# Performance work log

Measured on AMD Instinct MI355X. Metric: run time of the kernel, lower is better.

Reference implementation:

```python
import jax, jax.numpy as jnp
import numpy as np

D_MODEL = 1024
D_STATE = 64
D_CONV = 4
EXPAND = 2
HEADDIM = 64
FFN_MULT = 3
MEM_DIM = 256
D_INNER = EXPAND * D_MODEL            # 2048
NHEADS = D_INNER // HEADDIM           # 32
CONV_DIM = D_INNER + 2 * D_STATE      # x, B, C channels through the causal conv
D_IN_PROJ = 2 * D_INNER + 2 * D_STATE + NHEADS  # z, xBC, dt
FFN_HID = FFN_MULT * D_MODEL


def _rms(x, eps=1e-6):
    return x * jax.lax.rsqrt(jnp.mean(x * x, axis=-1, keepdims=True) + eps)


def _mamba2(u, in_proj_w, conv_w, conv_b, dt_bias, A_log, D_param, mnorm_w, out_proj_w):
    # u: [B, L, d_model]
    Bsz, L, _ = u.shape
    zxbcdt = u @ in_proj_w.T                                  # [B, L, D_IN_PROJ]
    z = zxbcdt[..., :D_INNER]                                 # gate branch
    xBC = zxbcdt[..., D_INNER:D_INNER + CONV_DIM]
    dt = zxbcdt[..., D_INNER + CONV_DIM:]                     # [B, L, H]
    # causal depthwise conv1d (kernel D_CONV) + silu
    xp = jnp.pad(xBC, ((0, 0), (D_CONV - 1, 0), (0, 0)))
    xBC = sum(xp[:, k:k + L, :] * conv_w[:, k] for k in range(D_CONV)) + conv_b
    xBC = jax.nn.silu(xBC)
    xh = xBC[..., :D_INNER].reshape(Bsz, L, NHEADS, HEADDIM)  # [B, L, H, P]
    Bm = xBC[..., D_INNER:D_INNER + D_STATE]                  # [B, L, N] (ngroups=1)
    Cm = xBC[..., D_INNER + D_STATE:]                         # [B, L, N]
    dt = jax.nn.softplus(dt + dt_bias)                        # [B, L, H]
    dA = jnp.exp(dt * (-jnp.exp(A_log)))                      # [B, L, H]

    def step(h, inp):
        # h: [B, H, P, N]
        da, dtt, xt, bt, ct = inp
        h = da[:, :, None, None] * h + jnp.einsum('bh,bhp,bn->bhpn', dtt, xt, bt)
        y = jnp.einsum('bhpn,bn->bhp', h, ct)
        return h, y

    h0 = jnp.zeros((Bsz, NHEADS, HEADDIM, D_STATE), u.dtype)
    xs = (jnp.moveaxis(dA, 1, 0), jnp.moveaxis(dt, 1, 0), jnp.moveaxis(xh, 1, 0),
          jnp.moveaxis(Bm, 1, 0), jnp.moveaxis(Cm, 1, 0))
    _, ys = jax.lax.scan(step, h0, xs)                        # ys: [L, B, H, P]
    y = jnp.moveaxis(ys, 0, 1) + D_param[None, None, :, None] * xh
    y = y.reshape(Bsz, L, D_INNER)
    y = _rms(y * jax.nn.silu(z)) * mnorm_w                    # RMSNormGated
    return y @ out_proj_w.T


def setup_inputs() -> dict:
    key = jax.random.key(0)
    ks = jax.random.split(key, 12)
    B, L = 1, 2048
    s = 0.02
    return {
        'x': jax.random.normal(ks[0], (B, L, D_MODEL), jnp.float32),
        'x0': jax.random.normal(ks[1], (B, L, D_MODEL), jnp.float32),
        'mem': jax.random.normal(ks[2], (B, MEM_DIM), jnp.float32),
        'resid_mix': jnp.stack([jnp.ones(D_MODEL), jnp.zeros(D_MODEL)]),
        'ssm_scale': jnp.ones(D_MODEL),
        'mlp_scale': jnp.ones(D_MODEL),
        'ssm_norm_w': jnp.ones(D_MODEL),
        'ffn_norm_w': jnp.ones(D_MODEL),
        'in_proj_w': jax.random.normal(ks[3], (D_IN_PROJ, D_MODEL), jnp.float32) * s,
        'conv_w': jax.random.normal(ks[4], (CONV_DIM, D_CONV), jnp.float32) * 0.2,
        'conv_b': jnp.zeros(CONV_DIM),
        'dt_bias': jax.random.uniform(ks[5], (NHEADS,), jnp.float32, -2.0, 0.0),
        'A_log': jnp.log(jnp.linspace(1.0, 16.0, NHEADS).astype(jnp.float32)),
        'D_param': jnp.ones(NHEADS),
        'mnorm_w': jnp.ones(D_INNER),
        'out_proj_w': jax.random.normal(ks[6], (D_MODEL, D_INNER), jnp.float32) * s,
        'gate_up_w': jax.random.normal(ks[7], (2 * FFN_HID, D_MODEL), jnp.float32) * s,
        'down_w': jax.random.normal(ks[8], (D_MODEL, FFN_HID), jnp.float32) * s,
    }


def reference(x, x0, mem, resid_mix, ssm_scale, mlp_scale, ssm_norm_w, ffn_norm_w,
              in_proj_w, conv_w, conv_b, dt_bias, A_log, D_param, mnorm_w,
              out_proj_w, gate_up_w, down_w):
    # residual mixing (USE_MEMORY=0, so mem path is inert)
    x = resid_mix[0][None, None, :] * x + resid_mix[1][None, None, :] * x0
    y = _mamba2(_rms(x) * ssm_norm_w, in_proj_w, conv_w, conv_b, dt_bias,
                A_log, D_param, mnorm_w, out_proj_w)
    x = x + ssm_scale[None, None, :] * y
    # SwiGLU FFN
    h = _rms(x) * ffn_norm_w
    gu = h @ gate_up_w.T
    gate, up = jnp.split(gu, 2, axis=-1)
    x = x + mlp_scale[None, None, :] * ((jax.nn.silu(gate) * up) @ down_w.T)
    return x
```

## Files before the change

kernel.cpp:

```cpp
#include <hip/hip_runtime.h>
#include <hip/hip_bf16.h>
#include <math.h>

#define LSEQ 2048
#define DMODEL 1024
#define DINNER 2048
#define NHEADS 32
#define HEADDIM 64
#define DSTATE 64
#define CONVDIM 2176
#define XBCDT_W 2304
#define FFNHID 3072

typedef float f32x4 __attribute__((ext_vector_type(4)));
typedef __bf16 bf16x8 __attribute__((ext_vector_type(8)));
typedef __hip_bfloat16 bf16;

__device__ __forceinline__ float siluf(float x){ return x / (1.0f + expf(-x)); }

#define GLOAD_LDS16(gp, lp) __builtin_amdgcn_global_load_lds( \
    (const __attribute__((address_space(1))) void*)(gp), \
    (__attribute__((address_space(3))) void*)(lp), 16, 0, 0)

__device__ __forceinline__ float block_reduce_sum_256(float v){
  #pragma unroll
  for (int o = 32; o > 0; o >>= 1) v += __shfl_down(v, o, 64);
  __shared__ float sh[4];
  int lane = threadIdx.x & 63;
  int w = threadIdx.x >> 6;
  if (lane == 0) sh[w] = v;
  __syncthreads();
  return sh[0] + sh[1] + sh[2] + sh[3];
}

__device__ __forceinline__ ushort bf16bits(float f){
  __hip_bfloat16 h = __float2bfloat16(f);
  return *reinterpret_cast<ushort*>(&h);
}
__device__ __forceinline__ float bfu(ushort u){
  union { float f; unsigned int i; } w; w.i = ((unsigned int)u) << 16; return w.f;
}

__device__ __forceinline__ int swz64(int r, int c){
  return r*64 + ((((c>>3) ^ (r&7)))<<3) + (c&7);
}

__global__ __launch_bounds__(256) void k_castmix(
    const float* __restrict__ w0, const float* __restrict__ w1,
    const float* __restrict__ w2, const float* __restrict__ w3,
    bf16* __restrict__ d0, bf16* __restrict__ d1,
    bf16* __restrict__ d2, bf16* __restrict__ d3,
    const float* __restrict__ x, const float* __restrict__ x0,
    const float* __restrict__ rm, const float* __restrict__ nw,
    float* __restrict__ xres, bf16* __restrict__ u)
{
  int tid = threadIdx.x;
  if (blockIdx.x < 15616){
    int idx = blockIdx.x * 256 + tid;
    const float* s; bf16* d; int valid;
    if (idx < 1114112)      { s = w0; d = d0; valid = 1089536; }
    else if (idx < 1638400) { idx -= 1114112; s = w1; d = d1; valid = 524288; }
    else if (idx < 3211264) { idx -= 1638400; s = w2; d = d2; valid = 1572864; }
    else                    { idx -= 3211264; s = w3; d = d3; valid = 786432; }
    float4 v = (idx < valid) ? *(const float4*)(s + (size_t)idx * 4)
                             : make_float4(0.f, 0.f, 0.f, 0.f);
    ushort4 r;
    r.x = bf16bits(v.x); r.y = bf16bits(v.y); r.z = bf16bits(v.z); r.w = bf16bits(v.w);
    *(ushort4*)(d + (size_t)idx * 4) = r;
    return;
  }
  int row = blockIdx.x - 15616;
  float4 xv  = ((const float4*)(x  + (size_t)row * DMODEL))[tid];
  float4 x0v = ((const float4*)(x0 + (size_t)row * DMODEL))[tid];
  float4 r0 = ((const float4*)rm)[tid];
  float4 r1 = ((const float4*)(rm + DMODEL))[tid];
  float4 a;
  a.x = r0.x*xv.x + r1.x*x0v.x; a.y = r0.y*xv.y + r1.y*x0v.y;
  a.z = r0.z*xv.z + r1.z*x0v.z; a.w = r0.w*xv.w + r1.w*x0v.w;
  ((float4*)(xres + (size_t)row * DMODEL))[tid] = a;
  float ss = a.x*a.x + a.y*a.y + a.z*a.z + a.w*a.w;
  ss = block_reduce_sum_256(ss);
  float inv = rsqrtf(ss / (float)DMODEL + 1e-6f);
  float4 nv = ((const float4*)nw)[tid];
  ushort4 o;
  o.x = bf16bits(a.x*inv*nv.x); o.y = bf16bits(a.y*inv*nv.y);
  o.z = bf16bits(a.z*inv*nv.z); o.w = bf16bits(a.w*inv*nv.w);
  *(ushort4*)(u + (size_t)row * DMODEL + tid*4) = o;
}

__device__ __forceinline__ void xcdswz2(int &bx, int &by){
  int gx = gridDim.x;
  int nblk = gx * gridDim.y;
  int flat = by * gx + bx;
  flat = (flat & 7) * (nblk >> 3) + (flat >> 3);
  by = flat / gx; bx = flat - by * gx;
}

__device__ __forceinline__ void gemm_mainloop128(
    const bf16* __restrict__ A, const bf16* __restrict__ W,
    int ld, int Klen, bf16* As, bf16* Ws, f32x4 acc[4][4])
{
  int tid = threadIdx.x, lane = tid & 63, wid = tid >> 6;
  int wm = (wid >> 1) * 64, wn = (wid & 1) * 64;
  int r16 = lane & 15, g8 = lane >> 4;
  int srow = lane >> 2;
  int scol = ((lane & 3) ^ (srow & 3) ^ ((srow >> 2) & 3)) * 8;
  const bf16* ga0 = A + (size_t)(wid*32 + srow) * ld + scol;
  const bf16* ga1 = ga0 + (size_t)16 * ld;
  const bf16* gw0 = W + (size_t)(wid*32 + srow) * ld + scol;
  const bf16* gw1 = gw0 + (size_t)16 * ld;
  GLOAD_LDS16(ga0, As + wid*1024);
  GLOAD_LDS16(ga1, As + wid*1024 + 512);
  GLOAD_LDS16(gw0, Ws + wid*1024);
  GLOAD_LDS16(gw1, Ws + wid*1024 + 512);
  __syncthreads();
  int cur = 0;
  int s4 = ((r16 & 3) ^ ((r16 >> 2) & 3)) * 8;
  for (int k0 = 0; k0 < Klen; k0 += 32){
    if (k0 + 32 < Klen){
      int nb = (cur ^ 1) * 4096;
      GLOAD_LDS16(ga0 + k0 + 32, As + nb + wid*1024);
      GLOAD_LDS16(ga1 + k0 + 32, As + nb + wid*1024 + 512);
      GLOAD_LDS16(gw0 + k0 + 32, Ws + nb + wid*1024);
      GLOAD_LDS16(gw1 + k0 + 32, Ws + nb + wid*1024 + 512);
    }
    int cb = cur * 4096;
    bf16x8 af[4], bfr[4];
    #pragma unroll
    for (int i = 0; i < 4; ++i)
      af[i] = *(const bf16x8*)(As + cb + (wm + i*16 + r16)*32 + (g8*8 ^ s4));
    #pragma unroll
    for (int j = 0; j < 4; ++j)
      bfr[j] = *(const bf16x8*)(Ws + cb + (wn + j*16 + r16)*32 + (g8*8 ^ s4));
    #pragma unroll
    for (int i = 0; i < 4; ++i)
      #pragma unroll
      for (int j = 0; j < 4; ++j)
        acc[i][j] = __builtin_amdgcn_mfma_f32_16x16x32_bf16(af[i], bfr[j], acc[i][j], 0, 0, 0);
    __syncthreads();
    cur ^= 1;
  }
}

__global__ __launch_bounds__(256) void k_gemm_inproj(
    const bf16* __restrict__ A, const bf16* __restrict__ Wfull,
    bf16* __restrict__ zbuf, bf16* __restrict__ xbcdt)
{
  __shared__ __align__(16) bf16 As[2*4096];
  __shared__ __align__(16) bf16 Ws[2*4096];
  int bx = blockIdx.x, by = blockIdx.y;
  xcdswz2(bx, by);
  f32x4 acc[4][4];
  #pragma unroll
  for (int i = 0; i < 4; ++i)
    #pragma unroll
    for (int j = 0; j < 4; ++j) acc[i][j] = (f32x4){0.f,0.f,0.f,0.f};
  gemm_mainloop128(A + (size_t)(by*128)*DMODEL, Wfull + (size_t)(bx*128)*DMODEL,
                   DMODEL, DMODEL, As, Ws, acc);
  int tid = threadIdx.x, lane = tid & 63, wid = tid >> 6;
  int wm = (wid >> 1) * 64, wn = (wid & 1) * 64;
  int r16 = lane & 15, g8 = lane >> 4;
  bf16* Cp; int ldc, col0;
  if (bx < 16){ Cp = zbuf;  ldc = DINNER;  col0 = bx*128; }
  else        { Cp = xbcdt; ldc = XBCDT_W; col0 = (bx-16)*128; }
  #pragma unroll
  for (int i = 0; i < 4; ++i){
    int row = by*128 + wm + i*16 + g8*4;
    #pragma unroll
    for (int j = 0; j < 4; ++j){
      int col = col0 + wn + j*16 + r16;
      #pragma unroll
      for (int r = 0; r < 4; ++r)
        Cp[(size_t)(row + r) * ldc + col] = __float2bfloat16(acc[i][j][r]);
    }
  }
}

__global__ __launch_bounds__(256) void k_gemm_splitk(
    const bf16* __restrict__ A, const bf16* __restrict__ W,
    bf16* __restrict__ P, int Kfull, int Kq, int N)
{
  __shared__ __align__(16) bf16 As[2*4096];
  __shared__ __align__(16) bf16 Ws[2*4096];
  int gx = gridDim.x, gxy = gx * gridDim.y;
  int nblk = gxy * gridDim.z;
  int flat = blockIdx.z * gxy + blockIdx.y * gx + blockIdx.x;
  flat = (flat & 7) * (nblk >> 3) + (flat >> 3);
  int z = flat / gxy; int rem = flat - z * gxy;
  int by = rem / gx, bx = rem - by * gx;
  f32x4 acc[4][4];
  #pragma unroll
  for (int i = 0; i < 4; ++i)
    #pragma unroll
    for (int j = 0; j < 4; ++j) acc[i][j] = (f32x4){0.f,0.f,0.f,0.f};
  gemm_mainloop128(A + (size_t)(by*128)*Kfull + z*Kq,
                   W + (size_t)(bx*128)*Kfull + z*Kq,
                   Kfull, Kq, As, Ws, acc);
  bf16* Pz = P + (size_t)z * LSEQ * N;
  int tid = threadIdx.x, lane = tid & 63, wid = tid >> 6;
  int wm = (wid >> 1) * 64, wn = (wid & 1) * 64;
  int r16 = lane & 15, g8 = lane >> 4;
  #pragma unroll
  for (int i = 0; i < 4; ++i){
    int row = by*128 + wm + i*16 + g8*4;
    #pragma unroll
    for (int j = 0; j < 4; ++j){
      int col = bx*128 + wn + j*16 + r16;
      #pragma unroll
      for (int r = 0; r < 4; ++r)
        Pz[(size_t)(row + r) * N + col] = __float2bfloat16(acc[i][j][r]);
    }
  }
}

__global__ __launch_bounds__(256) void k_gemm_ffn(
    const bf16* __restrict__ A, const bf16* __restrict__ Wg, const bf16* __restrict__ Wu,
    bf16* __restrict__ act, int K)
{
  __shared__ __align__(16) bf16 As[2*4096];
  __shared__ __align__(16) bf16 Ws[2*4096];
  int bx = blockIdx.x, by = blockIdx.y;
  xcdswz2(bx, by);
  int tid = threadIdx.x, lane = tid & 63, wid = tid >> 6;
  int wm = (wid >> 1) * 64, wc = (wid & 1) * 32;
  int r16 = lane & 15, g8 = lane >> 4;
  int srow = lane >> 2;
  int scol = ((lane & 3) ^ (srow & 3) ^ ((srow >> 2) & 3)) * 8;
  const bf16* ga0 = A + (size_t)(by*128 + wid*32 + srow) * K + scol;
  const bf16* ga1 = ga0 + (size_t)16 * K;
  const bf16* gwsrc = (wid < 2) ? Wg : Wu;
  const bf16* gw0 = gwsrc + (size_t)(bx*64 + (wid & 1)*32 + srow) * K + scol;
  const bf16* gw1 = gw0 + (size_t)16 * K;
  f32x4 accg[4][2], accu[4][2];
  #pragma unroll
  for (int i = 0; i < 4; ++i)
    #pragma unroll
    for (int j = 0; j < 2; ++j){
      accg[i][j] = (f32x4){0.f,0.f,0.f,0.f};
      accu[i][j] = (f32x4){0.f,0.f,0.f,0.f};
    }
  GLOAD_LDS16(ga0, As + wid*1024);
  GLOAD_LDS16(ga1, As + wid*1024 + 512);
  GLOAD_LDS16(gw0, Ws + wid*1024);
  GLOAD_LDS16(gw1, Ws + wid*1024 + 512);
  __syncthreads();
  int cur = 0;
  int s4 = ((r16 & 3) ^ ((r16 >> 2) & 3)) * 8;
  for (int k0 = 0; k0 < K; k0 += 32){
    if (k0 + 32 < K){
      int nb = (cur ^ 1) * 4096;
      GLOAD_LDS16(ga0 + k0 + 32, As + nb + wid*1024);
      GLOAD_LDS16(ga1 + k0 + 32, As + nb + wid*1024 + 512);
      GLOAD_LDS16(gw0 + k0 + 32, Ws + nb + wid*1024);
      GLOAD_LDS16(gw1 + k0 + 32, Ws + nb + wid*1024 + 512);
    }
    int cb = cur * 4096;
    bf16x8 af[4], gf[2], uf[2];
    #pragma unroll
    for (int i = 0; i < 4; ++i)
      af[i] = *(const bf16x8*)(As + cb + (wm + i*16 + r16)*32 + (g8*8 ^ s4));
    #pragma unroll
    for (int j = 0; j < 2; ++j){
      int gr = wc + j*16 + r16;
      int ur = 64 + wc + j*16 + r16;
      gf[j] = *(const bf16x8*)(Ws + cb + gr*32 + (g8*8 ^ s4));
      uf[j] = *(const bf16x8*)(Ws + cb + ur*32 + (g8*8 ^ s4));
    }
    #pragma unroll
    for (int i = 0; i < 4; ++i)
      #pragma unroll
      for (int j = 0; j < 2; ++j){
        accg[i][j] = __builtin_amdgcn_mfma_f32_16x16x32_bf16(af[i], gf[j], accg[i][j], 0, 0, 0);
        accu[i][j] = __builtin_amdgcn_mfma_f32_16x16x32_bf16(af[i], uf[j], accu[i][j], 0, 0, 0);
      }
    __syncthreads();
    cur ^= 1;
  }
  #pragma unroll
  for (int i = 0; i < 4; ++i){
    int row = by*128 + wm + i*16 + g8*4;
    #pragma unroll
    for (int j = 0; j < 2; ++j){
      int col = bx*64 + wc + j*16 + r16;
      #pragma unroll
      for (int r = 0; r < 4; ++r){
        float g = accg[i][j][r], u = accu[i][j][r];
        act[(size_t)(row + r) * FFNHID + col] = __float2bfloat16(siluf(g) * u);
      }
    }
  }
}

__global__ __launch_bounds__(256) void k_convdt(
    const bf16* __restrict__ xbcdt, const float* __restrict__ cw,
    const float* __restrict__ cb, const float* __restrict__ dtb,
    const float* __restrict__ alog, bf16* __restrict__ xbc,
    float* __restrict__ dtv, float* __restrict__ lav)
{
  int idx = blockIdx.x * 256 + threadIdx.x;
  int l = idx / 552, q = idx - l * 552;
  if (l >= LSEQ) return;
  if (q < 544){
    int c = q * 4;
    float4 bv = *(const float4*)(cb + c);
    float acc0 = bv.x, acc1 = bv.y, acc2 = bv.z, acc3 = bv.w;
    float4 w0 = *(const float4*)(cw + (size_t)(c+0)*4);
    float4 w1 = *(const float4*)(cw + (size_t)(c+1)*4);
    float4 w2 = *(const float4*)(cw + (size_t)(c+2)*4);
    float4 w3 = *(const float4*)(cw + (size_t)(c+3)*4);
    const float* w0p = (const float*)&w0;
    const float* w1p = (const float*)&w1;
    const float* w2p = (const float*)&w2;
    const float* w3p = (const float*)&w3;
    #pragma unroll
    for (int k = 0; k < 4; ++k){
      int t = l + k - 3;
      if (t < 0) continue;
      ushort4 rv = *(const ushort4*)(xbcdt + (size_t)t * XBCDT_W + c);
      acc0 = fmaf(bfu(rv.x), w0p[k], acc0);
      acc1 = fmaf(bfu(rv.y), w1p[k], acc1);
      acc2 = fmaf(bfu(rv.z), w2p[k], acc2);
      acc3 = fmaf(bfu(rv.w), w3p[k], acc3);
    }
    ushort4 o;
    o.x = bf16bits(siluf(acc0)); o.y = bf16bits(siluf(acc1));
    o.z = bf16bits(siluf(acc2)); o.w = bf16bits(siluf(acc3));
    *(ushort4*)(xbc + (size_t)l * CONVDIM + c) = o;
  } else {
    int h0 = (q - 544) * 4;
    ushort4 rv = *(const ushort4*)(xbcdt + (size_t)l * XBCDT_W + CONVDIM + h0);
    float raws[4] = { bfu(rv.x), bfu(rv.y), bfu(rv.z), bfu(rv.w) };
    #pragma unroll
    for (int i = 0; i < 4; ++i){
      float raw = raws[i] + dtb[h0 + i];
      float d = (raw > 20.f) ? raw : log1pf(expf(raw));
      dtv[l * NHEADS + h0 + i] = d;
      lav[l * NHEADS + h0 + i] = -expf(alog[h0 + i]) * d;
    }
  }
}

__global__ __launch_bounds__(256) void k_scanA(
    const bf16* __restrict__ xbc, const float* __restrict__ dtv,
    const float* __restrict__ lav, bf16* __restrict__ T, float* __restrict__ ctot)
{
  __shared__ __bf16 sXw[4096];
  __shared__ __bf16 sBt[4096];
  __shared__ float scum[64], swt[64];
  int h = blockIdx.x >> 5, c = blockIdx.x & 31;
  int tid = threadIdx.x, t0 = c * 64;
  if (tid < 64){
    float cum = lav[(size_t)(t0 + tid) * NHEADS + h];
    #pragma unroll
    for (int o = 1; o < 64; o <<= 1){
      float v = __shfl_up(cum, o, 64);
      if (tid >= o) cum += v;
    }
    scum[tid] = cum;
  }
  __syncthreads();
  float Lc = scum[63];
  if (tid < 64)
    swt[tid] = expf(Lc - scum[tid]) * dtv[(size_t)(t0 + tid) * NHEADS + h];
  __syncthreads();
  for (int idx = tid; idx < 512; idx += 256){
    int j = idx >> 3, n0 = (idx & 7) * 8;
    const bf16* rb = xbc + (size_t)(t0 + j) * CONVDIM;
    bf16x8 x8 = *(const bf16x8*)(rb + h * HEADDIM + n0);
    bf16x8 b8 = *(const bf16x8*)(rb + DINNER + n0);
    float wj = swt[j];
    #pragma unroll
    for (int e = 0; e < 8; ++e){
      sXw[swz64(n0 + e, j)] = (__bf16)((float)x8[e] * wj);
      sBt[swz64(n0 + e, j)] = b8[e];
    }
  }
  __syncthreads();
  int lane = tid & 63, wid = tid >> 6;
  int wr = (wid >> 1) * 32, wc = (wid & 1) * 32;
  int r16 = lane & 15, g8 = lane >> 4;
  f32x4 acc[2][2];
  #pragma unroll
  for (int i = 0; i < 2; ++i)
    #pragma unroll
    for (int j = 0; j < 2; ++j) acc[i][j] = (f32x4){0.f,0.f,0.f,0.f};
  #pragma unroll
  for (int kk = 0; kk < 2; ++kk){
    int ks = kk*4 + g8;
    bf16x8 a[2], b[2];
    #pragma unroll
    for (int i = 0; i < 2; ++i){
      int row = wr + i*16 + r16;
      a[i] = *(const bf16x8*)(sXw + row*64 + ((ks ^ (row&7))<<3));
    }
    #pragma unroll
    for (int j = 0; j < 2; ++j){
      int row = wc + j*16 + r16;
      b[j] = *(const bf16x8*)(sBt + row*64 + ((ks ^ (row&7))<<3));
    }
    #pragma unroll
    for (int i = 0; i < 2; ++i)
      #pragma unroll
      for (int j = 0; j < 2; ++j)
        acc[i][j] = __builtin_amdgcn_mfma_f32_16x16x32_bf16(a[i], b[j], acc[i][j], 0, 0, 0);
  }
  bf16* Tb = T + (size_t)blockIdx.x * 4096;
  #pragma unroll
  for (int i = 0; i < 2; ++i)
    #pragma unroll
    for (int j = 0; j < 2; ++j)
      #pragma unroll
      for (int r = 0; r < 4; ++r){
        int p = wr + i*16 + g8*4 + r, n = wc + j*16 + r16;
        Tb[p*64 + n] = __float2bfloat16(acc[i][j][r]);
      }
  if (tid == 0) ctot[blockIdx.x] = expf(Lc);
}

__global__ __launch_bounds__(256) void k_scanB(bf16* __restrict__ T, const float* __restrict__ ctot)
{
  int h = blockIdx.x >> 3, e = blockIdx.x & 7;
  int tid = threadIdx.x;
  size_t off = (size_t)e * 512 + tid * 2;
  float s0 = 0.f, s1 = 0.f;
  for (int c0 = 0; c0 < 32; c0 += 8){
    ushort2 tv[8]; float cts[8];
    #pragma unroll
    for (int q = 0; q < 8; ++q){
      cts[q] = ctot[h * 32 + c0 + q];
      tv[q] = *(const ushort2*)&T[(size_t)(h * 32 + c0 + q) * 4096 + off];
    }
    #pragma unroll
    for (int q = 0; q < 8; ++q){
      size_t base = (size_t)(h * 32 + c0 + q) * 4096 + off;
      ushort2 sv; sv.x = bf16bits(s0); sv.y = bf16bits(s1);
      *(ushort2*)&T[base] = sv;
      s0 = fmaf(cts[q], s0, bfu(tv[q].x));
      s1 = fmaf(cts[q], s1, bfu(tv[q].y));
    }
  }
}

__global__ __launch_bounds__(256) void k_scanC(
    const bf16* __restrict__ xbc, const bf16* __restrict__ Sin,
    const float* __restrict__ dtv, const float* __restrict__ lav,
    const float* __restrict__ Dp, bf16* __restrict__ y)
{
  __shared__ __bf16 sC[4096];
  __shared__ __bf16 sBS[4096];
  __shared__ __bf16 sXt[4096];
  __shared__ __bf16 sXr[4096];
  __shared__ __bf16 sSb[4096];
  __shared__ float scum[64], sdt[64];
  int h = blockIdx.x >> 5, c = blockIdx.x & 31;
  int tid = threadIdx.x, t0 = c * 64;
  if (tid < 64){
    float cum = lav[(size_t)(t0 + tid) * NHEADS + h];
    #pragma unroll
    for (int o = 1; o < 64; o <<= 1){
      float v = __shfl_up(cum, o, 64);
      if (tid >= o) cum += v;
    }
    scum[tid] = cum;
    sdt[tid] = dtv[(size_t)(t0 + tid) * NHEADS + h];
  }
  const bf16* Tb = Sin + (size_t)blockIdx.x * 4096;
  for (int idx = tid; idx < 512; idx += 256){
    int j = idx >> 3, n0 = (idx & 7) * 8;
    const bf16* rb = xbc + (size_t)(t0 + j) * CONVDIM;
    bf16x8 x8 = *(const bf16x8*)(rb + h * HEADDIM + n0);
    bf16x8 c8 = *(const bf16x8*)(rb + DINNER + DSTATE + n0);
    bf16x8 b8 = *(const bf16x8*)(rb + DINNER + n0);
    *(bf16x8*)(sC  + swz64(j, n0)) = c8;
    *(bf16x8*)(sBS + swz64(j, n0)) = b8;
    *(bf16x8*)(sXr + swz64(j, n0)) = x8;
    *(bf16x8*)(sSb + swz64(j, n0)) = *(const bf16x8*)(Tb + j*64 + n0);
    #pragma unroll
    for (int e = 0; e < 8; ++e)
      sXt[swz64(n0 + e, j)] = x8[e];
  }
  __syncthreads();
  int lane = tid & 63, wid = tid >> 6;
  int wr = (wid >> 1) * 32, wc = (wid & 1) * 32;
  int r16 = lane & 15, g8 = lane >> 4;
  f32x4 gacc[2][2];
  #pragma unroll
  for (int i = 0; i < 2; ++i)
    #pragma unroll
    for (int j = 0; j < 2; ++j) gacc[i][j] = (f32x4){0.f,0.f,0.f,0.f};
  #pragma unroll
  for (int kk = 0; kk < 2; ++kk){
    int ks = kk*4 + g8;
    bf16x8 a[2], b[2];
    #pragma unroll
    for (int i = 0; i < 2; ++i){
      int row = wr + i*16 + r16;
      a[i] = *(const bf16x8*)(sC + row*64 + ((ks ^ (row&7))<<3));
    }
    #pragma unroll
    for (int j = 0; j < 2; ++j){
      int row = wc + j*16 + r16;
      b[j] = *(const bf16x8*)(sBS + row*64 + ((ks ^ (row&7))<<3));
    }
    #pragma unroll
    for (int i = 0; i < 2; ++i)
      #pragma unroll
      for (int j = 0; j < 2; ++j)
        gacc[i][j] = __builtin_amdgcn_mfma_f32_16x16x32_bf16(a[i], b[j], gacc[i][j], 0, 0, 0);
  }
  __syncthreads();
  #pragma unroll
  for (int i = 0; i < 2; ++i)
    #pragma unroll
    for (int j = 0; j < 2; ++j)
      #pragma unroll
      for (int r = 0; r < 4; ++r){
        int i_ = wr + i*16 + g8*4 + r, j_ = wc + j*16 + r16;
        float v = (j_ <= i_) ? gacc[i][j][r] * expf(scum[i_] - scum[j_]) * sdt[j_] : 0.f;
        sBS[swz64(i_, j_)] = (__bf16)v;
      }
  __syncthreads();
  f32x4 a1[2][2], a2[2][2];
  #pragma unroll
  for (int i = 0; i < 2; ++i)
    #pragma unroll
    for (int j = 0; j < 2; ++j){
      a1[i][j] = (f32x4){0.f,0.f,0.f,0.f};
      a2[i][j] = (f32x4){0.f,0.f,0.f,0.f};
    }
  #pragma unroll
  for (int kk = 0; kk < 2; ++kk){
    int ks = kk*4 + g8;
    bf16x8 sa[2], xa[2], ca[2], sb[2];
    #pragma unroll
    for (int i = 0; i < 2; ++i){
      int row = wr + i*16 + r16;
      sa[i] = *(const bf16x8*)(sBS + row*64 + ((ks ^ (row&7))<<3));
      ca[i] = *(const bf16x8*)(sC  + row*64 + ((ks ^ (row&7))<<3));
    }
    #pragma unroll
    for (int j = 0; j < 2; ++j){
      int row = wc + j*16 + r16;
      xa[j] = *(const bf16x8*)(sXt + row*64 + ((ks ^ (row&7))<<3));
      sb[j] = *(const bf16x8*)(sSb + row*64 + ((ks ^ (row&7))<<3));
    }
    #pragma unroll
    for (int i = 0; i < 2; ++i)
      #pragma unroll
      for (int j = 0; j < 2; ++j){
        a1[i][j] = __builtin_amdgcn_mfma_f32_16x16x32_bf16(sa[i], xa[j], a1[i][j], 0, 0, 0);
        a2[i][j] = __builtin_amdgcn_mfma_f32_16x16x32_bf16(ca[i], sb[j], a2[i][j], 0, 0, 0);
      }
  }
  float Dh = Dp[h];
  #pragma unroll
  for (int i = 0; i < 2; ++i)
    #pragma unroll
    for (int r = 0; r < 4; ++r){
      int i_ = wr + i*16 + g8*4 + r;
      float wi = expf(scum[i_]);
      #pragma unroll
      for (int j = 0; j < 2; ++j){
        int p_ = wc + j*16 + r16;
        float xv = (float)sXr[swz64(i_, p_)];
        y[(size_t)(t0 + i_) * DINNER + h * HEADDIM + p_] =
            __float2bfloat16(a1[i][j][r] + wi * a2[i][j][r] + Dh * xv);
      }
    }
}

__global__ __launch_bounds__(256) void k_gate_rms(
    const bf16* __restrict__ y, const bf16* __restrict__ zbuf,
    const float* __restrict__ mw, bf16* __restrict__ yn)
{
  int row = blockIdx.x, tid = threadIdx.x;
  bf16x8 yv = *(const bf16x8*)(y    + (size_t)row * DINNER + tid*8);
  bf16x8 zv = *(const bf16x8*)(zbuf + (size_t)row * DINNER + tid*8);
  float g[8]; float ss = 0.f;
  #pragma unroll
  for (int e = 0; e < 8; ++e){
    float gv = (float)yv[e] * siluf((float)zv[e]);
    g[e] = gv; ss += gv * gv;
  }
  ss = block_reduce_sum_256(ss);
  float inv = rsqrtf(ss / (float)DINNER + 1e-6f);
  float4 m0 = ((const float4*)mw)[tid*2];
  float4 m1 = ((const float4*)mw)[tid*2 + 1];
  const float* mp = (const float*)&m0;
  bf16x8 o;
  #pragma unroll
  for (int e = 0; e < 4; ++e) o[e] = (__bf16)(g[e] * inv * mp[e]);
  mp = (const float*)&m1;
  #pragma unroll
  for (int e = 0; e < 4; ++e) o[4+e] = (__bf16)(g[4+e] * inv * mp[e]);
  *(bf16x8*)(yn + (size_t)row * DINNER + tid*8) = o;
}

__global__ __launch_bounds__(256) void k_res_rms(
    const float* __restrict__ xres, const bf16* __restrict__ yoP,
    const float* __restrict__ scale, const float* __restrict__ nw,
    float* __restrict__ x2, bf16* __restrict__ hb)
{
  int row = blockIdx.x, tid = threadIdx.x;
  const size_t PS = (size_t)LSEQ * DMODEL;
  float4 xv = ((const float4*)(xres + (size_t)row * DMODEL))[tid];
  ushort4 p0 = *(const ushort4*)(yoP          + (size_t)row * DMODEL + tid*4);
  ushort4 p1 = *(const ushort4*)(yoP +   PS   + (size_t)row * DMODEL + tid*4);
  ushort4 p2 = *(const ushort4*)(yoP + 2*PS   + (size_t)row * DMODEL + tid*4);
  ushort4 p3 = *(const ushort4*)(yoP + 3*PS   + (size_t)row * DMODEL + tid*4);
  float4 sv = ((const float4*)scale)[tid];
  float4 a;
  a.x = xv.x + sv.x*(bfu(p0.x)+bfu(p1.x)+bfu(p2.x)+bfu(p3.x));
  a.y = xv.y + sv.y*(bfu(p0.y)+bfu(p1.y)+bfu(p2.y)+bfu(p3.y));
  a.z = xv.z + sv.z*(bfu(p0.z)+bfu(p1.z)+bfu(p2.z)+bfu(p3.z));
  a.w = xv.w + sv.w*(bfu(p0.w)+bfu(p1.w)+bfu(p2.w)+bfu(p3.w));
  ((float4*)(x2 + (size_t)row * DMODEL))[tid] = a;
  float ss = a.x*a.x + a.y*a.y + a.z*a.z + a.w*a.w;
  ss = block_reduce_sum_256(ss);
  float inv = rsqrtf(ss / (float)DMODEL + 1e-6f);
  float4 nv = ((const float4*)nw)[tid];
  ushort4 o;
  o.x = bf16bits(a.x*inv*nv.x); o.y = bf16bits(a.y*inv*nv.y);
  o.z = bf16bits(a.z*inv*nv.z); o.w = bf16bits(a.w*inv*nv.w);
  *(ushort4*)(hb + (size_t)row * DMODEL + tid*4) = o;
}

__global__ __launch_bounds__(256) void k_final(
    const float* __restrict__ x2, const bf16* __restrict__ dP,
    const float* __restrict__ mscale, float* __restrict__ out)
{
  int i4 = blockIdx.x * 256 + threadIdx.x;
  const size_t PS = (size_t)LSEQ * DMODEL;
  float4 xv = ((const float4*)x2)[i4];
  ushort4 p0 = *(const ushort4*)(dP        + (size_t)i4*4);
  ushort4 p1 = *(const ushort4*)(dP + PS   + (size_t)i4*4);
  ushort4 p2 = *(const ushort4*)(dP + 2*PS + (size_t)i4*4);
  ushort4 p3 = *(const ushort4*)(dP + 3*PS + (size_t)i4*4);
  float4 mv = ((const float4*)mscale)[i4 & 255];
  float4 o;
  o.x = xv.x + mv.x*(bfu(p0.x)+bfu(p1.x)+bfu(p2.x)+bfu(p3.x));
  o.y = xv.y + mv.y*(bfu(p0.y)+bfu(p1.y)+bfu(p2.y)+bfu(p3.y));
  o.z = xv.z + mv.z*(bfu(p0.z)+bfu(p1.z)+bfu(p2.z)+bfu(p3.z));
  o.w = xv.w + mv.w*(bfu(p0.w)+bfu(p1.w)+bfu(p2.w)+bfu(p3.w));
  ((float4*)out)[i4] = o;
}

extern "C" void kernel_launch(void* const* d_in, const int* in_sizes, int n_in,
                              void* d_out, int out_size, void* d_ws, size_t ws_size,
                              hipStream_t stream)
{
  const float* x      = (const float*)d_in[0];
  const float* x0     = (const float*)d_in[1];
  const float* rm     = (const float*)d_in[3];
  const float* sscale = (const float*)d_in[4];
  const float* mscale = (const float*)d_in[5];
  const float* snw    = (const float*)d_in[6];
  const float* fnw    = (const float*)d_in[7];
  const float* win    = (const float*)d_in[8];
  const float* cw     = (const float*)d_in[9];
  const float* cb     = (const float*)d_in[10];
  const float* dtb    = (const float*)d_in[11];
  const float* alog   = (const float*)d_in[12];
  const float* Dp     = (const float*)d_in[13];
  const float* mnw    = (const float*)d_in[14];
  const float* wout   = (const float*)d_in[15];
  const float* wgu    = (const float*)d_in[16];
  const float* wdn    = (const float*)d_in[17];
  float* out = (float*)d_out;

  const size_t MB = 1024ull * 1024ull;
  char* ws = (char*)d_ws;
  bf16*  woutb = (bf16*) (ws + 0*MB);
  bf16*  wgub  = (bf16*) (ws + 4*MB);
  bf16*  wdnb  = (bf16*) (ws + 16*MB);
  float* xres  = (float*)(ws + 22*MB);
  bf16*  winb  = (bf16*) (ws + 30*MB);
  bf16*  u     = (bf16*) (ws + 39*MB);
  float* dtv   = (float*)(ws + 39*MB);
  float* lav   = (float*)(ws + 39*MB + 256*1024);
  bf16*  hb    = (bf16*) (ws + 39*MB);
  bf16*  zbuf  = (bf16*) (ws + 43*MB);
  float* x2    = (float*)(ws + 43*MB);
  bf16*  xbcdt = (bf16*) (ws + 59*MB);
  bf16*  yb    = (bf16*) (ws + 59*MB);
  bf16*  yoP   = (bf16*) (ws + 59*MB);
  bf16*  act   = (bf16*) (ws + 59*MB);
  bf16*  dP    = (bf16*) (ws + 71*MB);
  bf16*  xbc   = (bf16*) (ws + 77*MB);
  bf16*  T     = (bf16*) (ws + 95*MB);
  bf16*  yn    = (bf16*) (ws + 95*MB);
  float* ctot  = (float*)(ws + 112*MB);

  dim3 blk(256);
  k_castmix<<<17664, blk, 0, stream>>>(win, wout, wgu, wdn, winb, woutb, wgub, wdnb,
                                       x, x0, rm, snw, xres, u);
  k_gemm_inproj<<<dim3(34,16), blk, 0, stream>>>(u, winb, zbuf, xbcdt);
  k_convdt<<<(LSEQ*552)/256, blk, 0, stream>>>(xbcdt, cw, cb, dtb, alog, xbc, dtv, lav);
  k_scanA<<<NHEADS*32, blk, 0, stream>>>(xbc, dtv, lav, T, ctot);
  k_scanB<<<NHEADS*8, blk, 0, stream>>>(T, ctot);
  k_scanC<<<NHEADS*32, blk, 0, stream>>>(xbc, T, dtv, lav, Dp, yb);
  k_gate_rms<<<LSEQ, blk, 0, stream>>>(yb, zbuf, mnw, yn);
  k_gemm_splitk<<<dim3(8,16,4), blk, 0, stream>>>(yn, woutb, yoP, DINNER, DINNER/4, DMODEL);
  k_res_rms<<<LSEQ, blk, 0, stream>>>(xres, yoP, sscale, fnw, x2, hb);
  k_gemm_ffn<<<dim3(48,16), blk, 0, stream>>>(hb, wgub, wgub + (size_t)FFNHID*DMODEL, act, DMODEL);
  k_gemm_splitk<<<dim3(8,16,4), blk, 0, stream>>>(act, wdnb, dP, FFNHID, FFNHID/4, DMODEL);
  k_final<<<2048, blk, 0, stream>>>(x2, dP, mscale, out);
}
```

Measured before the change: 189.6 us.

## Fuse causal conv and dt softplus into scanA and scanC, drop conv kernel

After: 234.8 us. 1.24x slower.

```diff
diff --git a/kernel.cpp b/kernel.cpp
--- a/kernel.cpp
+++ b/kernel.cpp
@@ -43,6 +43,25 @@
 
 __device__ __forceinline__ int swz64(int r, int c){
   return r*64 + ((((c>>3) ^ (r&7)))<<3) + (c&7);
+}
+
+__device__ __forceinline__ void conv8(
+    const bf16* __restrict__ xbcdt, const float* __restrict__ cw,
+    const float* __restrict__ cb, int l, int c0, float out[8])
+{
+  #pragma unroll
+  for (int e = 0; e < 8; ++e) out[e] = cb[c0 + e];
+  #pragma unroll
+  for (int k = 0; k < 4; ++k){
+    int t = l + k - 3;
+    if (t < 0) continue;
+    bf16x8 rv = *(const bf16x8*)(xbcdt + (size_t)t * XBCDT_W + c0);
+    #pragma unroll
+    for (int e = 0; e < 8; ++e)
+      out[e] = fmaf((float)rv[e], cw[(c0 + e)*4 + k], out[e]);
+  }
+  #pragma unroll
+  for (int e = 0; e < 8; ++e) out[e] = siluf(out[e]);
 }
 
 __global__ __launch_bounds__(256) void k_castmix(
@@ -291,58 +310,10 @@
   }
 }
 
-__global__ __launch_bounds__(256) void k_convdt(
+__global__ __launch_bounds__(256) void k_scanA(
     const bf16* __restrict__ xbcdt, const float* __restrict__ cw,
     const float* __restrict__ cb, const float* __restrict__ dtb,
-    const float* __restrict__ alog, bf16* __restrict__ xbc,
-    float* __restrict__ dtv, float* __restrict__ lav)
-{
-  int idx = blockIdx.x * 256 + threadIdx.x;
-  int l = idx / 552, q = idx - l * 552;
-  if (l >= LSEQ) return;
-  if (q < 544){
-    int c = q * 4;
-    float4 bv = *(const float4*)(cb + c);
-    float acc0 = bv.x, acc1 = bv.y, acc2 = bv.z, acc3 = bv.w;
-    float4 w0 = *(const float4*)(cw + (size_t)(c+0)*4);
-    float4 w1 = *(const float4*)(cw + (size_t)(c+1)*4);
-    float4 w2 = *(const float4*)(cw + (size_t)(c+2)*4);
-    float4 w3 = *(const float4*)(cw + (size_t)(c+3)*4);
-    const float* w0p = (const float*)&w0;
-    const float* w1p = (const float*)&w1;
-    const float* w2p = (const float*)&w2;
-    const float* w3p = (const float*)&w3;
-    #pragma unroll
-    for (int k = 0; k < 4; ++k){
-      int t = l + k - 3;
-      if (t < 0) continue;
-      ushort4 rv = *(const ushort4*)(xbcdt + (size_t)t * XBCDT_W + c);
-      acc0 = fmaf(bfu(rv.x), w0p[k], acc0);
-      acc1 = fmaf(bfu(rv.y), w1p[k], acc1);
-      acc2 = fmaf(bfu(rv.z), w2p[k], acc2);
-      acc3 = fmaf(bfu(rv.w), w3p[k], acc3);
-    }
-    ushort4 o;
-    o.x = bf16bits(siluf(acc0)); o.y = bf16bits(siluf(acc1));
-    o.z = bf16bits(siluf(acc2)); o.w = bf16bits(siluf(acc3));
-    *(ushort4*)(xbc + (size_t)l * CONVDIM + c) = o;
-  } else {
-    int h0 = (q - 544) * 4;
-    ushort4 rv = *(const ushort4*)(xbcdt + (size_t)l * XBCDT_W + CONVDIM + h0);
-    float raws[4] = { bfu(rv.x), bfu(rv.y), bfu(rv.z), bfu(rv.w) };
-    #pragma unroll
-    for (int i = 0; i < 4; ++i){
-      float raw = raws[i] + dtb[h0 + i];
-      float d = (raw > 20.f) ? raw : log1pf(expf(raw));
-      dtv[l * NHEADS + h0 + i] = d;
-      lav[l * NHEADS + h0 + i] = -expf(alog[h0 + i]) * d;
-    }
-  }
-}
-
-__global__ __launch_bounds__(256) void k_scanA(
-    const bf16* __restrict__ xbc, const float* __restrict__ dtv,
-    const float* __restrict__ lav, bf16* __restrict__ T, float* __restrict__ ctot)
+    const float* __restrict__ alog, bf16* __restrict__ T, float* __restrict__ ctot)
 {
   __shared__ __bf16 sXw[4096];
   __shared__ __bf16 sBt[4096];
@@ -350,29 +321,35 @@
   int h = blockIdx.x >> 5, c = blockIdx.x & 31;
   int tid = threadIdx.x, t0 = c * 64;
   if (tid < 64){
-    float cum = lav[(size_t)(t0 + tid) * NHEADS + h];
+    int l = t0 + tid;
+    float raw = bfu(*(const ushort*)(xbcdt + (size_t)l * XBCDT_W + CONVDIM + h)) + dtb[h];
+    float d = (raw > 20.f) ? raw : log1pf(expf(raw));
+    float la = -expf(alog[h]) * d;
+    float cum = la;
     #pragma unroll
     for (int o = 1; o < 64; o <<= 1){
       float v = __shfl_up(cum, o, 64);
       if (tid >= o) cum += v;
     }
     scum[tid] = cum;
+    swt[tid] = d;
   }
   __syncthreads();
   float Lc = scum[63];
   if (tid < 64)
-    swt[tid] = expf(Lc - scum[tid]) * dtv[(size_t)(t0 + tid) * NHEADS + h];
+    swt[tid] = expf(Lc - scum[tid]) * swt[tid];
   __syncthreads();
   for (int idx = tid; idx < 512; idx += 256){
     int j = idx >> 3, n0 = (idx & 7) * 8;
-    const bf16* rb = xbc + (size_t)(t0 + j) * CONVDIM;
-    bf16x8 x8 = *(const bf16x8*)(rb + h * HEADDIM + n0);
-    bf16x8 b8 = *(const bf16x8*)(rb + DINNER + n0);
+    int l = t0 + j;
+    float xv[8], bv[8];
+    conv8(xbcdt, cw, cb, l, h * HEADDIM + n0, xv);
+    conv8(xbcdt, cw, cb, l, DINNER + n0, bv);
     float wj = swt[j];
     #pragma unroll
     for (int e = 0; e < 8; ++e){
-      sXw[swz64(n0 + e, j)] = (__bf16)((float)x8[e] * wj);
-      sBt[swz64(n0 + e, j)] = b8[e];
+      sXw[swz64(n0 + e, j)] = (__bf16)(xv[e] * wj);
+      sBt[swz64(n0 + e, j)] = (__bf16)bv[e];
     }
   }
   __syncthreads();
@@ -442,8 +419,9 @@
 }
 
 __global__ __launch_bounds__(256) void k_scanC(
-    const bf16* __restrict__ xbc, const bf16* __restrict__ Sin,
-    const float* __restrict__ dtv, const float* __restrict__ lav,
+    const bf16* __restrict__ xbcdt, const bf16* __restrict__ Sin,
+    const float* __restrict__ cw, const float* __restrict__ cb,
+    const float* __restrict__ dtb, const float* __restrict__ alog,
     const float* __restrict__ Dp, bf16* __restrict__ y)
 {
   __shared__ __bf16 sC[4096];
@@ -455,29 +433,35 @@
   int h = blockIdx.x >> 5, c = blockIdx.x & 31;
   int tid = threadIdx.x, t0 = c * 64;
   if (tid < 64){
-    float cum = lav[(size_t)(t0 + tid) * NHEADS + h];
+    int l = t0 + tid;
+    float raw = bfu(*(const ushort*)(xbcdt + (size_t)l * XBCDT_W + CONVDIM + h)) + dtb[h];
+    float d = (raw > 20.f) ? raw : log1pf(expf(raw));
+    float la = -expf(alog[h]) * d;
+    float cum = la;
     #pragma unroll
     for (int o = 1; o < 64; o <<= 1){
       float v = __shfl_up(cum, o, 64);
       if (tid >= o) cum += v;
     }
     scum[tid] = cum;
-    sdt[tid] = dtv[(size_t)(t0 + tid) * NHEADS + h];
+    sdt[tid] = d;
   }
   const bf16* Tb = Sin + (size_t)blockIdx.x * 4096;
   for (int idx = tid; idx < 512; idx += 256){
     int j = idx >> 3, n0 = (idx & 7) * 8;
-    const bf16* rb = xbc + (size_t)(t0 + j) * CONVDIM;
-    bf16x8 x8 = *(const bf16x8*)(rb + h * HEADDIM + n0);
-    bf16x8 c8 = *(const bf16x8*)(rb + DINNER + DSTATE + n0);
-    bf16x8 b8 = *(const bf16x8*)(rb + DINNER + n0);
-    *(bf16x8*)(sC  + swz64(j, n0)) = c8;
-    *(bf16x8*)(sBS + swz64(j, n0)) = b8;
-    *(bf16x8*)(sXr + swz64(j, n0)) = x8;
+    int l = t0 + j;
+    float xv[8], bv[8], cv[8];
+    conv8(xbcdt, cw, cb, l, h * HEADDIM + n0, xv);
+    conv8(xbcdt, cw, cb, l, DINNER + n0, bv);
+    conv8(xbcdt, cw, cb, l, DINNER + DSTATE + n0, cv);
+    #pragma unroll
+    for (int e = 0; e < 8; ++e){
+      sC [swz64(j, n0) + e] = (__bf16)cv[e];
+      sBS[swz64(j, n0) + e] = (__bf16)bv[e];
+      sXr[swz64(j, n0) + e] = (__bf16)xv[e];
+      sXt[swz64(n0 + e, j)] = (__bf16)xv[e];
+    }
     *(bf16x8*)(sSb + swz64(j, n0)) = *(const bf16x8*)(Tb + j*64 + n0);
-    #pragma unroll
-    for (int e = 0; e < 8; ++e)
-      sXt[swz64(n0 + e, j)] = x8[e];
   }
   __syncthreads();
   int lane = tid & 63, wid = tid >> 6;
@@ -676,29 +660,25 @@
   float* xres  = (float*)(ws + 22*MB);
   bf16*  winb  = (bf16*) (ws + 30*MB);
   bf16*  u     = (bf16*) (ws + 39*MB);
-  float* dtv   = (float*)(ws + 39*MB);
-  float* lav   = (float*)(ws + 39*MB + 256*1024);
   bf16*  hb    = (bf16*) (ws + 39*MB);
   bf16*  zbuf  = (bf16*) (ws + 43*MB);
   float* x2    = (float*)(ws + 43*MB);
   bf16*  xbcdt = (bf16*) (ws + 59*MB);
-  bf16*  yb    = (bf16*) (ws + 59*MB);
   bf16*  yoP   = (bf16*) (ws + 59*MB);
   bf16*  act   = (bf16*) (ws + 59*MB);
+  bf16*  yb    = (bf16*) (ws + 69*MB);
   bf16*  dP    = (bf16*) (ws + 71*MB);
-  bf16*  xbc   = (bf16*) (ws + 77*MB);
+  bf16*  yn    = (bf16*) (ws + 87*MB);
   bf16*  T     = (bf16*) (ws + 95*MB);
-  bf16*  yn    = (bf16*) (ws + 95*MB);
   float* ctot  = (float*)(ws + 112*MB);
 
   dim3 blk(256);
   k_castmix<<<17664, blk, 0, stream>>>(win, wout, wgu, wdn, winb, woutb, wgub, wdnb,
                                        x, x0, rm, snw, xres, u);
   k_gemm_inproj<<<dim3(34,16), blk, 0, stream>>>(u, winb, zbuf, xbcdt);
-  k_convdt<<<(LSEQ*552)/256, blk, 0, stream>>>(xbcdt, cw, cb, dtb, alog, xbc, dtv, lav);
-  k_scanA<<<NHEADS*32, blk, 0, stream>>>(xbc, dtv, lav, T, ctot);
+  k_scanA<<<NHEADS*32, blk, 0, stream>>>(xbcdt, cw, cb, dtb, alog, T, ctot);
   k_scanB<<<NHEADS*8, blk, 0, stream>>>(T, ctot);
-  k_scanC<<<NHEADS*32, blk, 0, stream>>>(xbc, T, dtv, lav, Dp, yb);
+  k_scanC<<<NHEADS*32, blk, 0, stream>>>(xbcdt, T, cw, cb, dtb, alog, Dp, yb);
   k_gate_rms<<<LSEQ, blk, 0, stream>>>(yb, zbuf, mnw, yn);
   k_gemm_splitk<<<dim3(8,16,4), blk, 0, stream>>>(yn, woutb, yoP, DINNER, DINNER/4, DMODEL);
   k_res_rms<<<LSEQ, blk, 0, stream>>>(xres, yoP, sscale, fnw, x2, hb);
```
